# Kernel tuning notes

Measured on AMD Instinct MI355X. Metric: run time of the kernel, lower is better.

Reference implementation:

```python
import math
import jax, jax.numpy as jnp
import numpy as np

N_EMBD = 1024
N_HEAD = 16
EPS = 1e-5


def get_alibi_slopes(n_head):
    def pow2_slopes(n):
        start = 2 ** (-2 ** (-(math.log2(n) - 3)))
        return [start * start ** i for i in range(n)]
    if math.log2(n_head).is_integer():
        slopes = pow2_slopes(n_head)
    else:
        c = 2 ** math.floor(math.log2(n_head))
        slopes = pow2_slopes(c)
        extra = pow2_slopes(2 * c)[0::2]
        slopes.extend(extra[: n_head - c])
    return jnp.asarray(slopes, dtype=jnp.float32)


def layernorm(x, w, b):
    mu = jnp.mean(x, axis=-1, keepdims=True)
    var = jnp.var(x, axis=-1, keepdims=True)
    return (x - mu) * jax.lax.rsqrt(var + EPS) * w + b


def setup_inputs() -> dict:
    key = jax.random.key(0)
    ks = jax.random.split(key, 8)
    C = N_EMBD
    B, T = 2, 2048
    s = 0.02
    return {
        "x": jax.random.normal(ks[0], (B, T, C), dtype=jnp.float32),
        "ln1_w": jnp.ones((C,), jnp.float32),
        "ln1_b": jnp.zeros((C,), jnp.float32),
        "w_qkv": jax.random.normal(ks[1], (C, 3 * C), dtype=jnp.float32) * s,
        "b_qkv": jnp.zeros((3 * C,), jnp.float32),
        "w_proj": jax.random.normal(ks[2], (C, C), dtype=jnp.float32) * s,
        "b_proj": jnp.zeros((C,), jnp.float32),
        "ln2_w": jnp.ones((C,), jnp.float32),
        "ln2_b": jnp.zeros((C,), jnp.float32),
        "w_fc": jax.random.normal(ks[3], (C, 4 * C), dtype=jnp.float32) * s,
        "b_fc": jnp.zeros((4 * C,), jnp.float32),
        "w_fc2": jax.random.normal(ks[4], (4 * C, C), dtype=jnp.float32) * s,
        "b_fc2": jnp.zeros((C,), jnp.float32),
    }


def reference(x, ln1_w, ln1_b, w_qkv, b_qkv, w_proj, b_proj,
              ln2_w, ln2_b, w_fc, b_fc, w_fc2, b_fc2):
    B, T, C = x.shape
    H = N_HEAD
    D = C // H

    # --- attention with ALiBi ---
    h = layernorm(x, ln1_w, ln1_b)
    qkv = h @ w_qkv + b_qkv                       # [B,T,3C]
    q, k, v = jnp.split(qkv, 3, axis=-1)
    q = q.reshape(B, T, H, D).transpose(0, 2, 1, 3)  # [B,H,T,D]
    k = k.reshape(B, T, H, D).transpose(0, 2, 1, 3)
    v = v.reshape(B, T, H, D).transpose(0, 2, 1, 3)

    att = jnp.einsum('bhqd,bhkd->bhqk', q, k) * (1.0 / math.sqrt(D))

    pos = jnp.arange(T, dtype=jnp.float32)
    distances = pos[:, None] - pos[None, :]        # [T,T], i-j
    slopes = get_alibi_slopes(H)[:, None, None]     # [H,1,1]
    bias = slopes * distances[None, :, :]           # [H,T,T]
    causal = jnp.triu(jnp.ones((T, T), dtype=bool), k=1)
    bias = jnp.where(causal[None, :, :], -jnp.inf, bias)

    att = jax.nn.softmax(att + bias[None], axis=-1)
    y = jnp.einsum('bhqk,bhkd->bhqd', att, v)
    y = y.transpose(0, 2, 1, 3).reshape(B, T, C)
    x = x + y @ w_proj + b_proj

    # --- MLP ---
    h = layernorm(x, ln2_w, ln2_b)
    h = jax.nn.gelu(h @ w_fc + b_fc, approximate=False)
    x = x + h @ w_fc2 + b_fc2
    return x
```

## Files before the change

kernel.cpp:

```cpp
#include <hip/hip_runtime.h>
#include <hip/hip_bf16.h>
#include <math.h>

#define N_EMBD 1024
#define N_HEADC 16
#define HEAD_D 64

typedef __attribute__((ext_vector_type(8))) short short8;
typedef __attribute__((ext_vector_type(4))) float floatx4;

__device__ __forceinline__ ushort f2b(float f) {
    __hip_bfloat16 h = __float2bfloat16(f);
    return *reinterpret_cast<ushort*>(&h);
}

__device__ __forceinline__ void async_cp16(const void* gsrc, void* ldst) {
    __builtin_amdgcn_global_load_lds(
        (const __attribute__((address_space(1))) void*)gsrc,
        (__attribute__((address_space(3))) void*)ldst, 16, 0, 0);
}

__device__ __forceinline__ int xcd_swizzle(int bid, int nwg) {
    const int q = nwg >> 3, r = nwg & 7;
    const int xcd = bid & 7, loc = bid >> 3;
    return (xcd < r ? xcd * (q + 1) : r * (q + 1) + (xcd - r) * q) + loc;
}

__global__ __launch_bounds__(256) void ln_kernel(const float* __restrict__ x,
                                                 const float* __restrict__ w,
                                                 const float* __restrict__ b,
                                                 ushort* __restrict__ out) {
    const int row = blockIdx.x;
    const int t = threadIdx.x;
    const float4 v = reinterpret_cast<const float4*>(x + (size_t)row * N_EMBD)[t];
    float s  = v.x + v.y + v.z + v.w;
    float ss = v.x * v.x + v.y * v.y + v.z * v.z + v.w * v.w;
    for (int o = 32; o > 0; o >>= 1) {
        s  += __shfl_down(s, o);
        ss += __shfl_down(ss, o);
    }
    __shared__ float as_[4], ass_[4];
    const int wid = t >> 6, lane = t & 63;
    if (lane == 0) { as_[wid] = s; ass_[wid] = ss; }
    __syncthreads();
    const float ts  = as_[0] + as_[1] + as_[2] + as_[3];
    const float tss = ass_[0] + ass_[1] + ass_[2] + ass_[3];
    const float mu  = ts * (1.f / N_EMBD);
    const float var = tss * (1.f / N_EMBD) - mu * mu;
    const float inv = rsqrtf(var + 1e-5f);
    const float4 wv = reinterpret_cast<const float4*>(w)[t];
    const float4 bv = reinterpret_cast<const float4*>(b)[t];
    ushort4 o;
    o.x = f2b((v.x - mu) * inv * wv.x + bv.x);
    o.y = f2b((v.y - mu) * inv * wv.y + bv.y);
    o.z = f2b((v.z - mu) * inv * wv.z + bv.z);
    o.w = f2b((v.w - mu) * inv * wv.w + bv.w);
    reinterpret_cast<ushort4*>(out + (size_t)row * N_EMBD)[t] = o;
}

__global__ void convtrans_kernel(const float* __restrict__ W,
                                 ushort* __restrict__ Wt, int K, int N) {
    __shared__ float tile[32][33];
    const int tid = threadIdx.x;
    const int r = tid >> 3;
    const int c4 = (tid & 7) * 4;
    const int bx = blockIdx.x, by = blockIdx.y;

    float4 v = *(const float4*)&W[((size_t)(by * 32 + r)) * N + bx * 32 + c4];
    tile[r][c4 + 0] = v.x; tile[r][c4 + 1] = v.y;
    tile[r][c4 + 2] = v.z; tile[r][c4 + 3] = v.w;
    __syncthreads();

    ushort4 u;
    u.x = f2b(tile[c4 + 0][r]); u.y = f2b(tile[c4 + 1][r]);
    u.z = f2b(tile[c4 + 2][r]); u.w = f2b(tile[c4 + 3][r]);
    *(ushort4*)&Wt[((size_t)(bx * 32 + r)) * K + by * 32 + c4] = u;
}

__device__ __forceinline__ void gemm_stage(
        const ushort* __restrict__ A, const ushort* __restrict__ Bt,
        ushort* As, ushort* Bs,
        int m0, int n0, int K, int k0, int w, int lane) {
#pragma unroll
    for (int l = 0; l < 2; l++) {
        const int cbase = w * 128 + l * 64;
        const int c = cbase + lane;
        const int row = c >> 2, kc8 = (c & 3) * 8;
        async_cp16(A  + (size_t)(m0 + row) * K + k0 + kc8, &As[cbase * 8]);
        async_cp16(Bt + (size_t)(n0 + row) * K + k0 + kc8, &Bs[cbase * 8]);
    }
}

__device__ __forceinline__ void gemm_compute(
        const ushort* As, const ushort* Bs, floatx4 (*acc)[4],
        int wm, int wn, int quad, int l16) {
    short8 a[4], bf[4];
#pragma unroll
    for (int i = 0; i < 4; i++)
        a[i] = *(const short8*)&As[(wm * 64 + i * 16 + l16) * 32 + quad * 8];
#pragma unroll
    for (int j = 0; j < 4; j++)
        bf[j] = *(const short8*)&Bs[(wn * 64 + j * 16 + l16) * 32 + quad * 8];
#pragma unroll
    for (int i = 0; i < 4; i++)
#pragma unroll
        for (int j = 0; j < 4; j++)
            acc[i][j] = __builtin_amdgcn_mfma_f32_16x16x32_bf16(
                a[i], bf[j], acc[i][j], 0, 0, 0);
}

__global__ __launch_bounds__(256) void gemm_bf16_kernel(
        const ushort* __restrict__ A,
        const ushort* __restrict__ Bt,
        const float* __restrict__ bias,
        const float* __restrict__ residual,
        float* __restrict__ out32,
        ushort* __restrict__ out16,
        int M, int N, int K, int do_gelu) {
    __shared__ ushort As[2][128 * 32];
    __shared__ ushort Bs[2][128 * 32];

    const int tid  = threadIdx.x;
    const int w    = tid >> 6;
    const int lane = tid & 63;
    const int quad = lane >> 4;
    const int l16  = lane & 15;
    const int wm   = w >> 1;
    const int wn   = w & 1;

    int bid = blockIdx.y * gridDim.x + blockIdx.x;
    bid = xcd_swizzle(bid, gridDim.x * gridDim.y);
    const int bx = bid % gridDim.x;
    const int by = bid / gridDim.x;
    const int m0 = by * 128;
    const int n0 = bx * 128;

    const int kchunk = K / gridDim.z;
    const int kbeg   = blockIdx.z * kchunk;
    if (gridDim.z > 1)
        out32 += (size_t)blockIdx.z * M * N;

    floatx4 acc[4][4];
#pragma unroll
    for (int i = 0; i < 4; i++)
#pragma unroll
        for (int j = 0; j < 4; j++) acc[i][j] = (floatx4){0.f, 0.f, 0.f, 0.f};

    const int nt = kchunk >> 5;

    gemm_stage(A, Bt, As[0], Bs[0], m0, n0, K, kbeg, w, lane);
    gemm_stage(A, Bt, As[1], Bs[1], m0, n0, K, kbeg + 32, w, lane);

    for (int t = 0; t < nt; t++) {
        if (t + 1 < nt) {
            asm volatile("s_waitcnt vmcnt(4)" ::: "memory");
        } else {
            asm volatile("s_waitcnt vmcnt(0)" ::: "memory");
        }
        __builtin_amdgcn_sched_barrier(0);
        __builtin_amdgcn_s_barrier();

        gemm_compute(As[t & 1], Bs[t & 1], acc, wm, wn, quad, l16);

        __builtin_amdgcn_s_barrier();
        if (t + 2 < nt)
            gemm_stage(A, Bt, As[t & 1], Bs[t & 1],
                       m0, n0, K, kbeg + ((t + 2) << 5), w, lane);
    }

#pragma unroll
    for (int i = 0; i < 4; i++) {
#pragma unroll
        for (int j = 0; j < 4; j++) {
            const int nn = n0 + wn * 64 + j * 16 + l16;
            const float bv = bias ? bias[nn] : 0.f;
#pragma unroll
            for (int r = 0; r < 4; r++) {
                const int mm = m0 + wm * 64 + i * 16 + quad * 4 + r;
                float v = acc[i][j][r] + bv;
                if (do_gelu) v = 0.5f * v * (1.f + erff(v * 0.70710678118654752f));
                if (residual) v += residual[(size_t)mm * N + nn];
                if (out32) out32[(size_t)mm * N + nn] = v;
                if (out16) out16[(size_t)mm * N + nn] = f2b(v);
            }
        }
    }
}

__global__ __launch_bounds__(256) void combine_kernel(
        const float* __restrict__ p0, const float* __restrict__ p1,
        const float* __restrict__ bias, float* __restrict__ out) {
    const int i = blockIdx.x * 256 + threadIdx.x;
    const float4 a = ((const float4*)p0)[i];
    const float4 c = ((const float4*)p1)[i];
    const float4 bb = ((const float4*)bias)[i & 255];
    float4 o = ((float4*)out)[i];
    o.x += a.x + c.x + bb.x;
    o.y += a.y + c.y + bb.y;
    o.z += a.z + c.z + bb.z;
    o.w += a.w + c.w + bb.w;
    ((float4*)out)[i] = o;
}

#define AT_PAD 72
#define LOG2E 1.4426950408889634f

__device__ __forceinline__ void attn_tile_step(
        short8 aq0, short8 aq1,
        ushort (*__restrict__ Ks)[AT_PAD],
        ushort (*__restrict__ Vt)[AT_PAD],
        ushort (*__restrict__ Ps)[AT_PAD],
        float& m_row, float& l_row, floatx4* acc,
        int qrow, int kt, bool domask,
        float qs2, float alibi_q, float skb16, const float* skq4,
        int w, int quad, int l16, int lane) {
    floatx4 sfrag[4];
#pragma unroll
    for (int kb = 0; kb < 4; kb++) {
        const int krow = kb * 16 + l16;
        short8 ak0 = *(const short8*)&Ks[krow][quad * 8];
        short8 ak1 = *(const short8*)&Ks[krow][32 + quad * 8];
        floatx4 s = (floatx4){0.f, 0.f, 0.f, 0.f};
        s = __builtin_amdgcn_mfma_f32_16x16x32_bf16(ak0, aq0, s, 0, 0, 0);
        s = __builtin_amdgcn_mfma_f32_16x16x32_bf16(ak1, aq1, s, 0, 0, 0);
        sfrag[kb] = s;
    }

    const float rowc = alibi_q - skb16 * (float)(kt * 4);
    float sv[4][4];
    float rm = -INFINITY;
#pragma unroll
    for (int kb = 0; kb < 4; kb++) {
        const float rck = rowc - skb16 * (float)kb;
#pragma unroll
        for (int r = 0; r < 4; r++) {
            float s = fmaf(sfrag[kb][r], qs2, rck - skq4[r]);
            if (domask) {
                const int k = kt * 64 + kb * 16 + quad * 4 + r;
                s = (k <= qrow) ? s : -INFINITY;
            }
            sv[kb][r] = s;
            rm = fmaxf(rm, s);
        }
    }
    rm = fmaxf(rm, __shfl_xor(rm, 16));
    rm = fmaxf(rm, __shfl_xor(rm, 32));

    if (__any(rm > m_row)) {
        const float mn = fmaxf(rm, m_row);
        const float corr = exp2f(m_row - mn);
        m_row = mn;
        l_row *= corr;
        float cr[4];
#pragma unroll
        for (int r = 0; r < 4; r++)
            cr[r] = __shfl(corr, (lane & 48) + quad * 4 + r);
#pragma unroll
        for (int db = 0; db < 4; db++)
#pragma unroll
            for (int r = 0; r < 4; r++) acc[db][r] *= cr[r];
    }

    float rs = 0.f;
#pragma unroll
    for (int kb = 0; kb < 4; kb++) {
        const float p0 = exp2f(sv[kb][0] - m_row);
        const float p1 = exp2f(sv[kb][1] - m_row);
        const float p2 = exp2f(sv[kb][2] - m_row);
        const float p3 = exp2f(sv[kb][3] - m_row);
        rs += (p0 + p1) + (p2 + p3);
        ushort4 pw;
        pw.x = f2b(p0); pw.y = f2b(p1); pw.z = f2b(p2); pw.w = f2b(p3);
        *(ushort4*)&Ps[w * 16 + l16][kb * 16 + quad * 4] = pw;
    }
    rs += __shfl_xor(rs, 16);
    rs += __shfl_xor(rs, 32);
    l_row += rs;

    short8 ap0 = *(const short8*)&Ps[w * 16 + l16][quad * 8];
    short8 ap1 = *(const short8*)&Ps[w * 16 + l16][32 + quad * 8];
#pragma unroll
    for (int db = 0; db < 4; db++) {
        const int dv = db * 16 + l16;
        const int svw = ((db * 4 + (l16 >> 2)) & 7) << 3;
        short8 bv0 = *(const short8*)&Vt[dv][(quad * 8) ^ svw];
        short8 bv1 = *(const short8*)&Vt[dv][(32 + quad * 8) ^ svw];
        acc[db] = __builtin_amdgcn_mfma_f32_16x16x32_bf16(ap0, bv0, acc[db], 0, 0, 0);
        acc[db] = __builtin_amdgcn_mfma_f32_16x16x32_bf16(ap1, bv1, acc[db], 0, 0, 0);
    }
}

__global__ __launch_bounds__(256) void attn_mfma_kernel(
        const ushort* __restrict__ qkv, ushort* __restrict__ y,
        float* __restrict__ opart, float* __restrict__ mpart,
        float* __restrict__ lpart, int B, int T) {
    const int C3 = 3 * N_EMBD;

    const int lin = xcd_swizzle(blockIdx.x, gridDim.x);
    const int bh = lin / 48;
    const int s  = lin % 48;
    int qt, cc, ktb_i, kte;
    bool split;
    if (s < 32) {
        split = true;
        qt = 31 - (s >> 1);
        cc = s & 1;
        const int hc = (qt + 2) >> 1;
        ktb_i = cc ? hc : 0;
        kte   = cc ? qt : hc - 1;
    } else {
        split = false;
        qt = 47 - s;
        cc = 0;
        ktb_i = 0;
        kte = qt;
    }
    const int b = bh >> 4, h = bh & 15;

    const int tid  = threadIdx.x;
    const int lane = tid & 63;
    const int w    = tid >> 6;
    const int quad = lane >> 4;
    const int l16  = lane & 15;

    __shared__ ushort QPs[64][AT_PAD];
    __shared__ ushort Ks[64][AT_PAD];
    __shared__ ushort Vt[64][AT_PAD];

    const float slope  = exp2f(-0.5f * (float)(h + 1));
    const float slope2 = slope * LOG2E;
    const float qs2    = 0.125f * LOG2E;

    const int q0 = qt * 64;
    const int qrow = q0 + w * 16 + l16;
    const float alibi_q = slope2 * (float)qrow;
    const float skb16   = slope2 * 16.f;
    float skq4[4];
#pragma unroll
    for (int r = 0; r < 4; r++) skq4[r] = slope2 * (float)(quad * 4 + r);

    const size_t hb = (size_t)b * T * C3 + (size_t)h * HEAD_D;

    int srow[4], sd0[4], svr[4];
#pragma unroll
    for (int i = 0; i < 4; i++) {
        const int idx = tid + i * 256;
        srow[i] = idx >> 4;
        sd0[i]  = (idx & 15) * 4;
        svr[i]  = srow[i] ^ ((idx & 7) << 3);
    }

#pragma unroll
    for (int i = 0; i < 4; i++) {
        *(ushort4*)&QPs[srow[i]][sd0[i]] =
            *(const ushort4*)&qkv[hb + (size_t)(q0 + srow[i]) * C3 + sd0[i]];
    }
    __syncthreads();

    const int mrow = w * 16 + l16;
    short8 aq0 = *(const short8*)&QPs[mrow][quad * 8];
    short8 aq1 = *(const short8*)&QPs[mrow][32 + quad * 8];

    float m_row = -INFINITY, l_row = 0.f;
    floatx4 acc[4];
#pragma unroll
    for (int r = 0; r < 4; r++) acc[r] = (floatx4){0.f, 0.f, 0.f, 0.f};

#pragma unroll
    for (int i = 0; i < 4; i++) {
        const size_t src = hb + (size_t)(ktb_i * 64 + srow[i]) * C3 + sd0[i];
        *(ushort4*)&Ks[srow[i]][sd0[i]] = *(const ushort4*)&qkv[src + N_EMBD];
        ushort4 vv = *(const ushort4*)&qkv[src + 2 * N_EMBD];
        Vt[sd0[i] + 0][svr[i]] = vv.x;
        Vt[sd0[i] + 1][svr[i]] = vv.y;
        Vt[sd0[i] + 2][svr[i]] = vv.z;
        Vt[sd0[i] + 3][svr[i]] = vv.w;
    }
    __syncthreads();

    for (int kt = ktb_i; kt <= kte; kt++) {
        ushort4 kreg[4], vreg[4];
        const bool pf = (kt < kte);
        if (pf) {
#pragma unroll
            for (int i = 0; i < 4; i++) {
                const size_t src =
                    hb + (size_t)((kt + 1) * 64 + srow[i]) * C3 + sd0[i];
                kreg[i] = *(const ushort4*)&qkv[src + N_EMBD];
                vreg[i] = *(const ushort4*)&qkv[src + 2 * N_EMBD];
            }
        }

        attn_tile_step(aq0, aq1, Ks, Vt, QPs, m_row, l_row, acc,
                       qrow, kt, kt == qt, qs2, alibi_q, skb16, skq4,
                       w, quad, l16, lane);
        __syncthreads();

        if (pf) {
#pragma unroll
            for (int i = 0; i < 4; i++) {
                *(ushort4*)&Ks[srow[i]][sd0[i]] = kreg[i];
                Vt[sd0[i] + 0][svr[i]] = vreg[i].x;
                Vt[sd0[i] + 1][svr[i]] = vreg[i].y;
                Vt[sd0[i] + 2][svr[i]] = vreg[i].z;
                Vt[sd0[i] + 3][svr[i]] = vreg[i].w;
            }
        }
        __syncthreads();
    }

    if (!split) {
        const float li = 1.f / l_row;
        float ia[4];
#pragma unroll
        for (int r = 0; r < 4; r++)
            ia[r] = __shfl(li, (lane & 48) + quad * 4 + r);
#pragma unroll
        for (int r = 0; r < 4; r++) {
            const int qa = q0 + w * 16 + quad * 4 + r;
#pragma unroll
            for (int db = 0; db < 4; db++) {
                y[((size_t)b * T + qa) * N_EMBD + h * HEAD_D + db * 16 + l16] =
                    f2b(acc[db][r] * ia[r]);
            }
        }
    } else {
        const int pidx = (bh * 16 + (qt - 16)) * 2 + cc;
#pragma unroll
        for (int r = 0; r < 4; r++) {
            const int row = w * 16 + quad * 4 + r;
#pragma unroll
            for (int db = 0; db < 4; db++) {
                opart[((size_t)pidx * 64 + row) * 64 + db * 16 + l16] =
                    acc[db][r];
            }
        }
        if (quad == 0) {
            mpart[pidx * 64 + w * 16 + l16] = m_row;
            lpart[pidx * 64 + w * 16 + l16] = l_row;
        }
    }
}

__global__ __launch_bounds__(256) void attn_combine_kernel(
        const float* __restrict__ opart, const float* __restrict__ mpart,
        const float* __restrict__ lpart, ushort* __restrict__ y, int T) {
    const int x  = blockIdx.x;
    const int bh = x >> 4;
    const int qt = 16 + (x & 15);
    const int b  = bh >> 4, h = bh & 15;
    const int t  = threadIdx.x;
    const int row = t >> 2;
    const int dq  = (t & 3) << 4;
    const int p0 = x * 2, p1 = p0 + 1;

    const float m0 = mpart[p0 * 64 + row], m1 = mpart[p1 * 64 + row];
    const float l0 = lpart[p0 * 64 + row], l1 = lpart[p1 * 64 + row];
    const float M  = fmaxf(m0, m1);
    const float w0 = exp2f(m0 - M), w1 = exp2f(m1 - M);
    const float inv = 1.f / (l0 * w0 + l1 * w1);

    const float* o0 = &opart[((size_t)p0 * 64 + row) * 64 + dq];
    const float* o1 = &opart[((size_t)p1 * 64 + row) * 64 + dq];
    ushort* yr = &y[((size_t)b * T + qt * 64 + row) * N_EMBD + h * HEAD_D + dq];
#pragma unroll
    for (int j = 0; j < 16; j += 4) {
        const float4 a = *(const float4*)&o0[j];
        const float4 c = *(const float4*)&o1[j];
        yr[j + 0] = f2b((a.x * w0 + c.x * w1) * inv);
        yr[j + 1] = f2b((a.y * w0 + c.y * w1) * inv);
        yr[j + 2] = f2b((a.z * w0 + c.z * w1) * inv);
        yr[j + 3] = f2b((a.w * w0 + c.w * w1) * inv);
    }
}

extern "C" void kernel_launch(void* const* d_in, const int* in_sizes, int n_in,
                              void* d_out, int out_size, void* d_ws, size_t ws_size,
                              hipStream_t stream) {
    const int B = 2, T = 2048, C = N_EMBD;
    const int M = B * T;

    const float* x      = (const float*)d_in[0];
    const float* ln1_w  = (const float*)d_in[1];
    const float* ln1_b  = (const float*)d_in[2];
    const float* w_qkv  = (const float*)d_in[3];
    const float* b_qkv  = (const float*)d_in[4];
    const float* w_proj = (const float*)d_in[5];
    const float* b_proj = (const float*)d_in[6];
    const float* ln2_w  = (const float*)d_in[7];
    const float* ln2_b  = (const float*)d_in[8];
    const float* w_fc   = (const float*)d_in[9];
    const float* b_fc   = (const float*)d_in[10];
    const float* w_fc2  = (const float*)d_in[11];
    const float* b_fc2  = (const float*)d_in[12];
    float* out = (float*)d_out;

    char* ws = (char*)d_ws;
    size_t off = 0;
    ushort* wt_qkv  = (ushort*)(ws + off); off += (size_t)3 * C * C * 2;
    ushort* wt_proj = (ushort*)(ws + off); off += (size_t)C * C * 2;
    ushort* wt_fc   = (ushort*)(ws + off); off += (size_t)4 * C * C * 2;
    ushort* wt_fc2  = (ushort*)(ws + off); off += (size_t)4 * C * C * 2;
    ushort* h16     = (ushort*)(ws + off); off += (size_t)M * C * 2;
    ushort* qkv16   = (ushort*)(ws + off); off += (size_t)M * 3 * C * 2;
    ushort* y16     = (ushort*)(ws + off); off += (size_t)M * C * 2;
    ushort* fc16    = (ushort*)(ws + off); off += (size_t)M * 4 * C * 2;

    convtrans_kernel<<<dim3(3 * C / 32, C / 32), 256, 0, stream>>>(w_qkv, wt_qkv, C, 3 * C);
    convtrans_kernel<<<dim3(C / 32, C / 32), 256, 0, stream>>>(w_proj, wt_proj, C, C);
    convtrans_kernel<<<dim3(4 * C / 32, C / 32), 256, 0, stream>>>(w_fc, wt_fc, C, 4 * C);
    convtrans_kernel<<<dim3(C / 32, 4 * C / 32), 256, 0, stream>>>(w_fc2, wt_fc2, 4 * C, C);

    ln_kernel<<<M, 256, 0, stream>>>(x, ln1_w, ln1_b, h16);

    gemm_bf16_kernel<<<dim3(3 * C / 128, M / 128), 256, 0, stream>>>(
        h16, wt_qkv, b_qkv, nullptr, nullptr, qkv16, M, 3 * C, C, 0);

    float* aop = (float*)fc16;
    float* amp = aop + (size_t)1024 * 64 * 64;
    float* alp = amp + (size_t)1024 * 64;
    attn_mfma_kernel<<<32 * 48, 256, 0, stream>>>(
        qkv16, y16, aop, amp, alp, B, T);
    attn_combine_kernel<<<512, 256, 0, stream>>>(aop, amp, alp, y16, T);

    gemm_bf16_kernel<<<dim3(C / 128, M / 128), 256, 0, stream>>>(
        y16, wt_proj, b_proj, x, out, nullptr, M, C, C, 0);

    ln_kernel<<<M, 256, 0, stream>>>(out, ln2_w, ln2_b, h16);

    gemm_bf16_kernel<<<dim3(4 * C / 128, M / 128), 256, 0, stream>>>(
        h16, wt_fc, b_fc, nullptr, nullptr, fc16, M, 4 * C, C, 1);

    float* part = (float*)h16;
    gemm_bf16_kernel<<<dim3(C / 128, M / 128, 2), 256, 0, stream>>>(
        fc16, wt_fc2, nullptr, nullptr, part, nullptr, M, C, 4 * C, 0);
    combine_kernel<<<(M * C) / (256 * 4), 256, 0, stream>>>(
        part, part + (size_t)M * C, b_fc2, out);
}
```

Baseline: 409.3 us.

## Add 256x256-tile 512-thread bf16 GEMM with swizzled LDS for large GEMMs

```diff
diff --git a/kernel.cpp b/kernel.cpp
--- a/kernel.cpp
+++ b/kernel.cpp
@@ -25,6 +25,8 @@
     const int xcd = bid & 7, loc = bid >> 3;
     return (xcd < r ? xcd * (q + 1) : r * (q + 1) + (xcd - r) * q) + loc;
 }
+
+__device__ __forceinline__ int swzkey(int row) { return ((row >> 1) & 3) << 3; }
 
 __global__ __launch_bounds__(256) void ln_kernel(const float* __restrict__ x,
                                                  const float* __restrict__ w,
@@ -177,6 +179,121 @@
 #pragma unroll
             for (int r = 0; r < 4; r++) {
                 const int mm = m0 + wm * 64 + i * 16 + quad * 4 + r;
+                float v = acc[i][j][r] + bv;
+                if (do_gelu) v = 0.5f * v * (1.f + erff(v * 0.70710678118654752f));
+                if (residual) v += residual[(size_t)mm * N + nn];
+                if (out32) out32[(size_t)mm * N + nn] = v;
+                if (out16) out16[(size_t)mm * N + nn] = f2b(v);
+            }
+        }
+    }
+}
+
+__device__ __forceinline__ void gemm256_stage(
+        const ushort* __restrict__ A, const ushort* __restrict__ Bt,
+        ushort* As, ushort* Bs,
+        int m0, int n0, int K, int k0, int w, int lane) {
+#pragma unroll
+    for (int l = 0; l < 2; l++) {
+        const int cbase = l * 512 + w * 64;
+        const int c = cbase + lane;
+        const int row = c >> 2;
+        const int gcol = ((c & 3) * 8) ^ swzkey(row);
+        async_cp16(A  + (size_t)(m0 + row) * K + k0 + gcol, &As[cbase * 8]);
+        async_cp16(Bt + (size_t)(n0 + row) * K + k0 + gcol, &Bs[cbase * 8]);
+    }
+}
+
+__device__ __forceinline__ void gemm256_compute(
+        const ushort* As, const ushort* Bs, floatx4 (*acc)[4],
+        int wr, int wc, int quad, int l16) {
+    short8 a[8], b[4];
+#pragma unroll
+    for (int i = 0; i < 8; i++) {
+        const int row = wr * 128 + i * 16 + l16;
+        a[i] = *(const short8*)&As[row * 32 + ((quad * 8) ^ swzkey(row))];
+    }
+#pragma unroll
+    for (int j = 0; j < 4; j++) {
+        const int row = wc * 64 + j * 16 + l16;
+        b[j] = *(const short8*)&Bs[row * 32 + ((quad * 8) ^ swzkey(row))];
+    }
+#pragma unroll
+    for (int i = 0; i < 8; i++)
+#pragma unroll
+        for (int j = 0; j < 4; j++)
+            acc[i][j] = __builtin_amdgcn_mfma_f32_16x16x32_bf16(
+                a[i], b[j], acc[i][j], 0, 0, 0);
+}
+
+__global__ __launch_bounds__(512, 2) void gemm256_bf16_kernel(
+        const ushort* __restrict__ A,
+        const ushort* __restrict__ Bt,
+        const float* __restrict__ bias,
+        const float* __restrict__ residual,
+        float* __restrict__ out32,
+        ushort* __restrict__ out16,
+        int M, int N, int K, int do_gelu) {
+    __shared__ ushort As[2][256 * 32];
+    __shared__ ushort Bs[2][256 * 32];
+
+    const int tid  = threadIdx.x;
+    const int w    = tid >> 6;
+    const int lane = tid & 63;
+    const int quad = lane >> 4;
+    const int l16  = lane & 15;
+    const int wr   = w >> 2;
+    const int wc   = w & 3;
+
+    int bid = blockIdx.y * gridDim.x + blockIdx.x;
+    bid = xcd_swizzle(bid, gridDim.x * gridDim.y);
+    const int bx = bid % gridDim.x;
+    const int by = bid / gridDim.x;
+    const int m0 = by * 256;
+    const int n0 = bx * 256;
+
+    const int kchunk = K / gridDim.z;
+    const int kbeg   = blockIdx.z * kchunk;
+    if (gridDim.z > 1)
+        out32 += (size_t)blockIdx.z * M * N;
+
+    floatx4 acc[8][4];
+#pragma unroll
+    for (int i = 0; i < 8; i++)
+#pragma unroll
+        for (int j = 0; j < 4; j++) acc[i][j] = (floatx4){0.f, 0.f, 0.f, 0.f};
+
+    const int nt = kchunk >> 5;
+
+    gemm256_stage(A, Bt, As[0], Bs[0], m0, n0, K, kbeg, w, lane);
+    gemm256_stage(A, Bt, As[1], Bs[1], m0, n0, K, kbeg + 32, w, lane);
+
+    for (int t = 0; t < nt; t++) {
+        if (t + 1 < nt) {
+            asm volatile("s_waitcnt vmcnt(4)" ::: "memory");
+        } else {
+            asm volatile("s_waitcnt vmcnt(0)" ::: "memory");
+        }
+        __builtin_amdgcn_sched_barrier(0);
+        __builtin_amdgcn_s_barrier();
+
+        gemm256_compute(As[t & 1], Bs[t & 1], acc, wr, wc, quad, l16);
+
+        __builtin_amdgcn_s_barrier();
+        if (t + 2 < nt)
+            gemm256_stage(A, Bt, As[t & 1], Bs[t & 1],
+                          m0, n0, K, kbeg + ((t + 2) << 5), w, lane);
+    }
+
+#pragma unroll
+    for (int i = 0; i < 8; i++) {
+#pragma unroll
+        for (int j = 0; j < 4; j++) {
+            const int nn = n0 + wc * 64 + j * 16 + l16;
+            const float bv = bias ? bias[nn] : 0.f;
+#pragma unroll
+            for (int r = 0; r < 4; r++) {
+                const int mm = m0 + wr * 128 + i * 16 + quad * 4 + r;
                 float v = acc[i][j][r] + bv;
                 if (do_gelu) v = 0.5f * v * (1.f + erff(v * 0.70710678118654752f));
                 if (residual) v += residual[(size_t)mm * N + nn];
@@ -513,7 +630,7 @@
 
     ln_kernel<<<M, 256, 0, stream>>>(x, ln1_w, ln1_b, h16);
 
-    gemm_bf16_kernel<<<dim3(3 * C / 128, M / 128), 256, 0, stream>>>(
+    gemm256_bf16_kernel<<<dim3(3 * C / 256, M / 256), 512, 0, stream>>>(
         h16, wt_qkv, b_qkv, nullptr, nullptr, qkv16, M, 3 * C, C, 0);
 
     float* aop = (float*)fc16;
@@ -528,11 +645,11 @@
 
     ln_kernel<<<M, 256, 0, stream>>>(out, ln2_w, ln2_b, h16);
 
-    gemm_bf16_kernel<<<dim3(4 * C / 128, M / 128), 256, 0, stream>>>(
+    gemm256_bf16_kernel<<<dim3(4 * C / 256, M / 256), 512, 0, stream>>>(
         h16, wt_fc, b_fc, nullptr, nullptr, fc16, M, 4 * C, C, 1);
 
     float* part = (float*)h16;
-    gemm_bf16_kernel<<<dim3(C / 128, M / 128, 2), 256, 0, stream>>>(
+    gemm256_bf16_kernel<<<dim3(C / 256, M / 256, 2), 512, 0, stream>>>(
         fc16, wt_fc2, nullptr, nullptr, part, nullptr, M, C, 4 * C, 0);
     combine_kernel<<<(M * C) / (256 * 4), 256, 0, stream>>>(
         part, part + (size_t)M * C, b_fc2, out);
```

New measurement: 449.4 us. 1.1x slower.

## Split-K the projection GEMM and use 64-deep K tiles for FC2

Applied to the files above, without the earlier changes.

```diff
diff --git a/kernel.cpp b/kernel.cpp
--- a/kernel.cpp
+++ b/kernel.cpp
@@ -109,6 +109,29 @@
                 a[i], bf[j], acc[i][j], 0, 0, 0);
 }
 
+__device__ __forceinline__ void gemm_epilogue(
+        floatx4 (*acc)[4], const float* bias, const float* residual,
+        float* out32, ushort* out16, int M, int N,
+        int m0, int n0, int wm, int wn, int quad, int l16, int do_gelu) {
+#pragma unroll
+    for (int i = 0; i < 4; i++) {
+#pragma unroll
+        for (int j = 0; j < 4; j++) {
+            const int nn = n0 + wn * 64 + j * 16 + l16;
+            const float bv = bias ? bias[nn] : 0.f;
+#pragma unroll
+            for (int r = 0; r < 4; r++) {
+                const int mm = m0 + wm * 64 + i * 16 + quad * 4 + r;
+                float v = acc[i][j][r] + bv;
+                if (do_gelu) v = 0.5f * v * (1.f + erff(v * 0.70710678118654752f));
+                if (residual) v += residual[(size_t)mm * N + nn];
+                if (out32) out32[(size_t)mm * N + nn] = v;
+                if (out16) out16[(size_t)mm * N + nn] = f2b(v);
+            }
+        }
+    }
+}
+
 __global__ __launch_bounds__(256) void gemm_bf16_kernel(
         const ushort* __restrict__ A,
         const ushort* __restrict__ Bt,
@@ -168,37 +191,89 @@
                        m0, n0, K, kbeg + ((t + 2) << 5), w, lane);
     }
 
-#pragma unroll
-    for (int i = 0; i < 4; i++) {
-#pragma unroll
-        for (int j = 0; j < 4; j++) {
-            const int nn = n0 + wn * 64 + j * 16 + l16;
-            const float bv = bias ? bias[nn] : 0.f;
-#pragma unroll
-            for (int r = 0; r < 4; r++) {
-                const int mm = m0 + wm * 64 + i * 16 + quad * 4 + r;
-                float v = acc[i][j][r] + bv;
-                if (do_gelu) v = 0.5f * v * (1.f + erff(v * 0.70710678118654752f));
-                if (residual) v += residual[(size_t)mm * N + nn];
-                if (out32) out32[(size_t)mm * N + nn] = v;
-                if (out16) out16[(size_t)mm * N + nn] = f2b(v);
-            }
-        }
-    }
+    gemm_epilogue(acc, bias, residual, out32, out16, M, N,
+                  m0, n0, wm, wn, quad, l16, do_gelu);
+}
+
+__global__ __launch_bounds__(256) void gemm_bf16_k64_kernel(
+        const ushort* __restrict__ A,
+        const ushort* __restrict__ Bt,
+        float* __restrict__ out32,
+        int M, int N, int K) {
+    __shared__ ushort As[2][2 * 128 * 32];
+    __shared__ ushort Bs[2][2 * 128 * 32];
+
+    const int tid  = threadIdx.x;
+    const int w    = tid >> 6;
+    const int lane = tid & 63;
+    const int quad = lane >> 4;
+    const int l16  = lane & 15;
+    const int wm   = w >> 1;
+    const int wn   = w & 1;
+
+    int bid = blockIdx.y * gridDim.x + blockIdx.x;
+    bid = xcd_swizzle(bid, gridDim.x * gridDim.y);
+    const int bx = bid % gridDim.x;
+    const int by = bid / gridDim.x;
+    const int m0 = by * 128;
+    const int n0 = bx * 128;
+
+    const int kchunk = K / gridDim.z;
+    const int kbeg   = blockIdx.z * kchunk;
+    if (gridDim.z > 1)
+        out32 += (size_t)blockIdx.z * M * N;
+
+    floatx4 acc[4][4];
+#pragma unroll
+    for (int i = 0; i < 4; i++)
+#pragma unroll
+        for (int j = 0; j < 4; j++) acc[i][j] = (floatx4){0.f, 0.f, 0.f, 0.f};
+
+    const int nt = kchunk >> 6;
+
+    gemm_stage(A, Bt, As[0],        Bs[0],        m0, n0, K, kbeg,      w, lane);
+    gemm_stage(A, Bt, As[0] + 4096, Bs[0] + 4096, m0, n0, K, kbeg + 32, w, lane);
+    gemm_stage(A, Bt, As[1],        Bs[1],        m0, n0, K, kbeg + 64, w, lane);
+    gemm_stage(A, Bt, As[1] + 4096, Bs[1] + 4096, m0, n0, K, kbeg + 96, w, lane);
+
+    for (int t = 0; t < nt; t++) {
+        if (t + 1 < nt) {
+            asm volatile("s_waitcnt vmcnt(8)" ::: "memory");
+        } else {
+            asm volatile("s_waitcnt vmcnt(0)" ::: "memory");
+        }
+        __builtin_amdgcn_sched_barrier(0);
+        __builtin_amdgcn_s_barrier();
+
+        gemm_compute(As[t & 1],        Bs[t & 1],        acc, wm, wn, quad, l16);
+        gemm_compute(As[t & 1] + 4096, Bs[t & 1] + 4096, acc, wm, wn, quad, l16);
+
+        __builtin_amdgcn_s_barrier();
+        if (t + 2 < nt) {
+            const int k2 = kbeg + ((t + 2) << 6);
+            gemm_stage(A, Bt, As[t & 1],        Bs[t & 1],        m0, n0, K, k2,      w, lane);
+            gemm_stage(A, Bt, As[t & 1] + 4096, Bs[t & 1] + 4096, m0, n0, K, k2 + 32, w, lane);
+        }
+    }
+
+    gemm_epilogue(acc, nullptr, nullptr, out32, nullptr, M, N,
+                  m0, n0, wm, wn, quad, l16, 0);
 }
 
 __global__ __launch_bounds__(256) void combine_kernel(
         const float* __restrict__ p0, const float* __restrict__ p1,
-        const float* __restrict__ bias, float* __restrict__ out) {
+        const float* __restrict__ bias, const float* __restrict__ res,
+        float* __restrict__ out) {
     const int i = blockIdx.x * 256 + threadIdx.x;
     const float4 a = ((const float4*)p0)[i];
     const float4 c = ((const float4*)p1)[i];
     const float4 bb = ((const float4*)bias)[i & 255];
-    float4 o = ((float4*)out)[i];
-    o.x += a.x + c.x + bb.x;
-    o.y += a.y + c.y + bb.y;
-    o.z += a.z + c.z + bb.z;
-    o.w += a.w + c.w + bb.w;
+    const float4 rr = ((const float4*)res)[i];
+    float4 o;
+    o.x = rr.x + a.x + c.x + bb.x;
+    o.y = rr.y + a.y + c.y + bb.y;
+    o.z = rr.z + a.z + c.z + bb.z;
+    o.w = rr.w + a.w + c.w + bb.w;
     ((float4*)out)[i] = o;
 }
 
@@ -523,8 +598,11 @@
         qkv16, y16, aop, amp, alp, B, T);
     attn_combine_kernel<<<512, 256, 0, stream>>>(aop, amp, alp, y16, T);
 
-    gemm_bf16_kernel<<<dim3(C / 128, M / 128), 256, 0, stream>>>(
-        y16, wt_proj, b_proj, x, out, nullptr, M, C, C, 0);
+    float* pp = (float*)h16;
+    gemm_bf16_kernel<<<dim3(C / 128, M / 128, 2), 256, 0, stream>>>(
+        y16, wt_proj, nullptr, nullptr, pp, nullptr, M, C, C, 0);
+    combine_kernel<<<(M * C) / (256 * 4), 256, 0, stream>>>(
+        pp, pp + (size_t)M * C, b_proj, x, out);
 
     ln_kernel<<<M, 256, 0, stream>>>(out, ln2_w, ln2_b, h16);
 
@@ -532,8 +610,8 @@
         h16, wt_fc, b_fc, nullptr, nullptr, fc16, M, 4 * C, C, 1);
 
     float* part = (float*)h16;
-    gemm_bf16_kernel<<<dim3(C / 128, M / 128, 2), 256, 0, stream>>>(
-        fc16, wt_fc2, nullptr, nullptr, part, nullptr, M, C, 4 * C, 0);
+    gemm_bf16_k64_kernel<<<dim3(C / 128, M / 128, 2), 256, 0, stream>>>(
+        fc16, wt_fc2, part, M, C, 4 * C);
     combine_kernel<<<(M * C) / (256 * 4), 256, 0, stream>>>(
-        part, part + (size_t)M * C, b_fc2, out);
-}
+        part, part + (size_t)M * C, b_fc2, out, out);
+}
```

Result: faster. 396.4 us (-3.2%).
